# Kernel optimization log

Measured on AMD Instinct MI355X. Metric: run time of the kernel, lower is better.

## Reference

```python
import jax, jax.numpy as jnp
import numpy as np

# Tokenizer hyperparams (match init_kwargs)
NUM_VARS = 8
EMBED = 64
WIN = 16
STEP = 4
SWIDTH = 1.0  # sample_width
PWIDTH = 1.0  # patch_width
BATCH = 32
SAMPLES = 4096


def setup_inputs() -> dict:
    key = jax.random.key(0)
    k1, k2, k3, k4, k5 = jax.random.split(key, 5)
    return {
        "x": jax.random.normal(k1, (BATCH, NUM_VARS, SAMPLES), dtype=jnp.float32),
        "W1": jax.random.normal(k2, (NUM_VARS, EMBED), dtype=jnp.float32),   # sample-level LSH hyperplanes
        "b1": jax.random.normal(k3, (EMBED,), dtype=jnp.float32),
        "W2": jax.random.normal(k4, (WIN * EMBED, EMBED), dtype=jnp.float32),  # patch-level LSH hyperplanes
        "b2": jax.random.normal(k5, (EMBED,), dtype=jnp.float32),
    }


def reference(x, W1, b1, W2, b2):
    B, V, S = x.shape
    # encode(): per-timestep sample-level LSH hash, fully vectorized over S.
    # torch loop does sample_level(x[:,:,ix]) for each ix -> one batched einsum here.
    # e: [B, EMBED, S]
    e = jnp.floor((jnp.einsum('bvs,vd->bds', x, W1) + b1[None, :, None]) / SWIDTH)

    # quantize(): sliding windows over the time axis.
    starts = jnp.arange(0, S - WIN, STEP)                 # [T] window start positions
    idx = starts[:, None] + jnp.arange(WIN)[None, :]
    wins = e[:, :, idx]
    T = starts.shape[0]
    flat = wins.transpose(0, 2, 1, 3).reshape(B, T, EMBED * WIN)
    # patch-level LSH hash per window
    tokens = jnp.floor((jnp.einsum('btf,fe->bte', flat, W2) + b2) / PWIDTH)  # [B, T, EMBED]
    return tokens
```

## Files before the change

kernel.cpp:

```cpp
#include <hip/hip_runtime.h>
#include <cstdint>
#include <cstddef>

#define B_ 32
#define V_ 8
#define S_ 4096
#define E_ 64
#define T_ 1020
#define TT 32
#define SLP 200

typedef __bf16 bf16_t;
typedef bf16_t bf16x8 __attribute__((ext_vector_type(8)));
typedef float f32x4 __attribute__((ext_vector_type(4)));

__global__ __launch_bounds__(256) void prep_kernel(const float* __restrict__ W2,
                                                   bf16_t* __restrict__ w2sw) {
  const int q = blockIdx.x * 256 + threadIdx.x;
  const int l = q & 63, nt = (q >> 6) & 3, kk = q >> 8;
  const int fb = kk * 32 + (l >> 4) * 8;
  const int n = nt * 16 + (l & 15);
  bf16x8 v;
#pragma unroll
  for (int j = 0; j < 8; ++j) v[j] = (bf16_t)W2[(fb + j) * E_ + n];
  *reinterpret_cast<bf16x8*>(w2sw + (size_t)q * 8) = v;
}

__global__ __launch_bounds__(256, 4) void fused_kernel(const float* __restrict__ x,
                                                       const float* __restrict__ W1,
                                                       const float* __restrict__ b1,
                                                       const bf16_t* __restrict__ w2sw,
                                                       const float* __restrict__ b2,
                                                       float* __restrict__ out) {
  __shared__ bf16_t et[E_ * SLP];
  const int tid = threadIdx.x;
  const int b = blockIdx.y;
  const int t0 = blockIdx.x * TT;
  {
    const int dg = tid >> 5;
    const int sg = tid & 31;
    const int s0 = 4 * t0;
    float xv[V_][5];
#pragma unroll
    for (int v = 0; v < V_; ++v) {
#pragma unroll
      for (int k = 0; k < 5; ++k) {
        int s = s0 + sg + 32 * k;
        if (s > S_ - 1) s = S_ - 1;
        xv[v][k] = x[((size_t)(b * V_ + v) << 12) + s];
      }
    }
#pragma unroll
    for (int dd = 0; dd < 8; ++dd) {
      const int d = dg * 8 + dd;
      const float bb = b1[d];
      float acc[5];
#pragma unroll
      for (int k = 0; k < 5; ++k) acc[k] = bb;
#pragma unroll
      for (int v = 0; v < V_; ++v) {
        const float w = W1[v * E_ + d];
#pragma unroll
        for (int k = 0; k < 5; ++k) acc[k] += xv[v][k] * w;
      }
#pragma unroll
      for (int k = 0; k < 5; ++k)
        et[d * SLP + sg + 32 * k] = (bf16_t)floorf(acc[k]);
    }
  }
  __syncthreads();
  const int lane = tid & 63;
  const int wv = tid >> 6;
  const int l15 = lane & 15;
  const int g = lane >> 4;
  const char* etb = reinterpret_cast<const char*>(et);
  const uint32_t aoff = 400u * (g >> 1) + 8u * l15 + 16u * (g & 1);
  const bf16_t* bptr = w2sw + (((size_t)wv * 64 + lane) << 3);
  const float bv = b2[wv * 16 + l15];
  f32x4 acc0 = {bv, bv, bv, bv};
  f32x4 acc1 = {bv, bv, bv, bv};
#pragma unroll 4
  for (int kk = 0; kk < 32; ++kk) {
    const char* pa = etb + aoff + 800 * kk;
    union { uint64_t q[2]; bf16x8 v; } A0, A1;
    A0.q[0] = *reinterpret_cast<const uint64_t*>(pa);
    A0.q[1] = *reinterpret_cast<const uint64_t*>(pa + 8);
    A1.q[0] = *reinterpret_cast<const uint64_t*>(pa + 128);
    A1.q[1] = *reinterpret_cast<const uint64_t*>(pa + 136);
    const bf16x8 Bf = *reinterpret_cast<const bf16x8*>(bptr + ((size_t)kk << 11));
    acc0 = __builtin_amdgcn_mfma_f32_16x16x32_bf16(A0.v, Bf, acc0, 0, 0, 0);
    acc1 = __builtin_amdgcn_mfma_f32_16x16x32_bf16(A1.v, Bf, acc1, 0, 0, 0);
  }
#pragma unroll
  for (int r = 0; r < 4; ++r) {
    const int t1 = t0 + g * 4 + r;
    if (t1 < T_) out[((size_t)(b * T_ + t1)) * E_ + wv * 16 + l15] = floorf(acc0[r]);
    const int t2 = t0 + 16 + g * 4 + r;
    if (t2 < T_) out[((size_t)(b * T_ + t2)) * E_ + wv * 16 + l15] = floorf(acc1[r]);
  }
}

extern "C" void kernel_launch(void* const* d_in, const int* in_sizes, int n_in,
                              void* d_out, int out_size, void* d_ws, size_t ws_size,
                              hipStream_t stream) {
  const float* x  = (const float*)d_in[0];
  const float* W1 = (const float*)d_in[1];
  const float* b1 = (const float*)d_in[2];
  const float* W2 = (const float*)d_in[3];
  const float* b2 = (const float*)d_in[4];
  float* out = (float*)d_out;

  bf16_t* w2sw = (bf16_t*)d_ws;

  hipLaunchKernelGGL(prep_kernel, dim3(32), dim3(256), 0, stream, W2, w2sw);
  hipLaunchKernelGGL(fused_kernel, dim3((T_ + TT - 1) / TT, B_), dim3(256), 0, stream,
                     x, W1, b1, w2sw, b2, out);
}
```

Measured before the change: 21.35 us.

## Use 32x32x16 MFMA with split-K across waves and LDS reduction

```diff
diff --git a/kernel.cpp b/kernel.cpp
--- a/kernel.cpp
+++ b/kernel.cpp
@@ -12,14 +12,14 @@
 
 typedef __bf16 bf16_t;
 typedef bf16_t bf16x8 __attribute__((ext_vector_type(8)));
-typedef float f32x4 __attribute__((ext_vector_type(4)));
+typedef float f32x16 __attribute__((ext_vector_type(16)));
 
 __global__ __launch_bounds__(256) void prep_kernel(const float* __restrict__ W2,
                                                    bf16_t* __restrict__ w2sw) {
   const int q = blockIdx.x * 256 + threadIdx.x;
-  const int l = q & 63, nt = (q >> 6) & 3, kk = q >> 8;
-  const int fb = kk * 32 + (l >> 4) * 8;
-  const int n = nt * 16 + (l & 15);
+  const int l = q & 63, nh = (q >> 6) & 1, kk = q >> 7;
+  const int fb = 16 * kk + 8 * (l >> 5);
+  const int n = 32 * nh + (l & 31);
   bf16x8 v;
 #pragma unroll
   for (int j = 0; j < 8; ++j) v[j] = (bf16_t)W2[(fb + j) * E_ + n];
@@ -71,32 +71,44 @@
   __syncthreads();
   const int lane = tid & 63;
   const int wv = tid >> 6;
-  const int l15 = lane & 15;
-  const int g = lane >> 4;
+  const int nh = wv & 1;
+  const int kh = wv >> 1;
+  const int l31 = lane & 31;
+  const int g = lane >> 5;
   const char* etb = reinterpret_cast<const char*>(et);
-  const uint32_t aoff = 400u * (g >> 1) + 8u * l15 + 16u * (g & 1);
-  const bf16_t* bptr = w2sw + (((size_t)wv * 64 + lane) << 3);
-  const float bv = b2[wv * 16 + l15];
-  f32x4 acc0 = {bv, bv, bv, bv};
-  f32x4 acc1 = {bv, bv, bv, bv};
-#pragma unroll 4
-  for (int kk = 0; kk < 32; ++kk) {
-    const char* pa = etb + aoff + 800 * kk;
-    union { uint64_t q[2]; bf16x8 v; } A0, A1;
-    A0.q[0] = *reinterpret_cast<const uint64_t*>(pa);
-    A0.q[1] = *reinterpret_cast<const uint64_t*>(pa + 8);
-    A1.q[0] = *reinterpret_cast<const uint64_t*>(pa + 128);
-    A1.q[1] = *reinterpret_cast<const uint64_t*>(pa + 136);
-    const bf16x8 Bf = *reinterpret_cast<const bf16x8*>(bptr + ((size_t)kk << 11));
-    acc0 = __builtin_amdgcn_mfma_f32_16x16x32_bf16(A0.v, Bf, acc0, 0, 0, 0);
-    acc1 = __builtin_amdgcn_mfma_f32_16x16x32_bf16(A1.v, Bf, acc1, 0, 0, 0);
+  const uint32_t aoff = 8u * l31 + 16u * g + 400u * (kh * 32);
+  const bf16_t* bptr = w2sw + ((size_t)kh * 32768 + nh * 512 + lane * 8);
+  f32x16 acc = {};
+#pragma unroll 8
+  for (int kkl = 0; kkl < 32; ++kkl) {
+    const char* pa = etb + aoff + 400u * kkl;
+    union { uint64_t q[2]; bf16x8 v; } A;
+    A.q[0] = *reinterpret_cast<const uint64_t*>(pa);
+    A.q[1] = *reinterpret_cast<const uint64_t*>(pa + 8);
+    const bf16x8 Bf = *reinterpret_cast<const bf16x8*>(bptr + ((size_t)kkl << 10));
+    acc = __builtin_amdgcn_mfma_f32_32x32x16_bf16(A.v, Bf, acc, 0, 0, 0);
   }
+  __syncthreads();
+  float* red = reinterpret_cast<float*>(et);
+  if (kh == 1) {
 #pragma unroll
-  for (int r = 0; r < 4; ++r) {
-    const int t1 = t0 + g * 4 + r;
-    if (t1 < T_) out[((size_t)(b * T_ + t1)) * E_ + wv * 16 + l15] = floorf(acc0[r]);
-    const int t2 = t0 + 16 + g * 4 + r;
-    if (t2 < T_) out[((size_t)(b * T_ + t2)) * E_ + wv * 16 + l15] = floorf(acc1[r]);
+    for (int r = 0; r < 16; ++r) red[r * 128 + nh * 64 + lane] = acc[r];
+  }
+  __syncthreads();
+  if (kh == 0) {
+    const float bv = b2[nh * 32 + l31];
+#pragma unroll
+    for (int r = 0; r < 16; ++r) acc[r] += red[r * 128 + nh * 64 + lane];
+#pragma unroll
+    for (int q4 = 0; q4 < 4; ++q4) {
+#pragma unroll
+      for (int rr = 0; rr < 4; ++rr) {
+        const int row = q4 * 8 + rr + 4 * g;
+        const int t = t0 + row;
+        if (t < T_)
+          out[((size_t)(b * T_ + t)) * E_ + nh * 32 + l31] = floorf(acc[q4 * 4 + rr] + bv);
+      }
+    }
   }
 }
 
```

Result: slower. 22.36 us (+4.7%).

## Prefetch W2 fragments into registers before stage 1 and remap sample-hash threads

Applied to the files above, without the earlier changes.

```diff
diff --git a/kernel.cpp b/kernel.cpp
--- a/kernel.cpp
+++ b/kernel.cpp
@@ -13,6 +13,8 @@
 typedef __bf16 bf16_t;
 typedef bf16_t bf16x8 __attribute__((ext_vector_type(8)));
 typedef float f32x4 __attribute__((ext_vector_type(4)));
+typedef unsigned long long u64;
+typedef u64 u64x2 __attribute__((ext_vector_type(2)));
 
 __global__ __launch_bounds__(256) void prep_kernel(const float* __restrict__ W2,
                                                    bf16_t* __restrict__ w2sw) {
@@ -36,57 +38,80 @@
   const int tid = threadIdx.x;
   const int b = blockIdx.y;
   const int t0 = blockIdx.x * TT;
-  {
-    const int dg = tid >> 5;
-    const int sg = tid & 31;
-    const int s0 = 4 * t0;
-    float xv[V_][5];
+  const int lane = tid & 63;
+  const int wvu = __builtin_amdgcn_readfirstlane(tid >> 6);
+  const int l15 = lane & 15;
+  const int g = lane >> 4;
+  const int s0 = 4 * t0;
+
+  int sc[3];
+#pragma unroll
+  for (int k = 0; k < 3; ++k) {
+    int s = s0 + lane + 64 * k;
+    sc[k] = (s > S_ - 1) ? (S_ - 1) : s;
+  }
+  float xv[V_][3];
+#pragma unroll
+  for (int v = 0; v < V_; ++v) {
+    const float* xb = x + ((size_t)(b * V_ + v) << 12);
+#pragma unroll
+    for (int k = 0; k < 3; ++k) xv[v][k] = xb[sc[k]];
+  }
+  const bf16_t* bptr = w2sw + (((size_t)wvu * 64 + lane) << 3);
+  bf16x8 bpre[16];
+#pragma unroll
+  for (int kk = 0; kk < 16; ++kk) {
+    bpre[kk] = *reinterpret_cast<const bf16x8*>(bptr + ((size_t)kk << 11));
+    u64x2 t = __builtin_bit_cast(u64x2, bpre[kk]);
+    asm volatile("" : "+v"(t[0]), "+v"(t[1]));
+    bpre[kk] = __builtin_bit_cast(bf16x8, t);
+  }
+
+  const int dbase = wvu * 16;
+  const float* w1w = W1 + dbase;
+  const float* b1w = b1 + dbase;
+#pragma unroll
+  for (int dd = 0; dd < 16; ++dd) {
+    const float bb = b1w[dd];
+    float a0 = bb, a1 = bb, a2 = bb;
 #pragma unroll
     for (int v = 0; v < V_; ++v) {
-#pragma unroll
-      for (int k = 0; k < 5; ++k) {
-        int s = s0 + sg + 32 * k;
-        if (s > S_ - 1) s = S_ - 1;
-        xv[v][k] = x[((size_t)(b * V_ + v) << 12) + s];
-      }
+      const float w = w1w[v * E_ + dd];
+      a0 += xv[v][0] * w;
+      a1 += xv[v][1] * w;
+      a2 += xv[v][2] * w;
     }
-#pragma unroll
-    for (int dd = 0; dd < 8; ++dd) {
-      const int d = dg * 8 + dd;
-      const float bb = b1[d];
-      float acc[5];
-#pragma unroll
-      for (int k = 0; k < 5; ++k) acc[k] = bb;
-#pragma unroll
-      for (int v = 0; v < V_; ++v) {
-        const float w = W1[v * E_ + d];
-#pragma unroll
-        for (int k = 0; k < 5; ++k) acc[k] += xv[v][k] * w;
-      }
-#pragma unroll
-      for (int k = 0; k < 5; ++k)
-        et[d * SLP + sg + 32 * k] = (bf16_t)floorf(acc[k]);
-    }
+    const int row = (dbase + dd) * SLP;
+    et[row + lane]      = (bf16_t)floorf(a0);
+    et[row + lane + 64] = (bf16_t)floorf(a1);
+    if (lane < 12) et[row + lane + 128] = (bf16_t)floorf(a2);
   }
   __syncthreads();
-  const int lane = tid & 63;
-  const int wv = tid >> 6;
-  const int l15 = lane & 15;
-  const int g = lane >> 4;
+
   const char* etb = reinterpret_cast<const char*>(et);
   const uint32_t aoff = 400u * (g >> 1) + 8u * l15 + 16u * (g & 1);
-  const bf16_t* bptr = w2sw + (((size_t)wv * 64 + lane) << 3);
-  const float bv = b2[wv * 16 + l15];
+  const float bv = b2[wvu * 16 + l15];
   f32x4 acc0 = {bv, bv, bv, bv};
   f32x4 acc1 = {bv, bv, bv, bv};
-#pragma unroll 4
-  for (int kk = 0; kk < 32; ++kk) {
+#pragma unroll
+  for (int kk = 0; kk < 16; ++kk) {
     const char* pa = etb + aoff + 800 * kk;
-    union { uint64_t q[2]; bf16x8 v; } A0, A1;
-    A0.q[0] = *reinterpret_cast<const uint64_t*>(pa);
-    A0.q[1] = *reinterpret_cast<const uint64_t*>(pa + 8);
-    A1.q[0] = *reinterpret_cast<const uint64_t*>(pa + 128);
-    A1.q[1] = *reinterpret_cast<const uint64_t*>(pa + 136);
+    union { u64 q[2]; bf16x8 v; } A0, A1;
+    A0.q[0] = *reinterpret_cast<const u64*>(pa);
+    A0.q[1] = *reinterpret_cast<const u64*>(pa + 8);
+    A1.q[0] = *reinterpret_cast<const u64*>(pa + 128);
+    A1.q[1] = *reinterpret_cast<const u64*>(pa + 136);
+    acc0 = __builtin_amdgcn_mfma_f32_16x16x32_bf16(A0.v, bpre[kk], acc0, 0, 0, 0);
+    acc1 = __builtin_amdgcn_mfma_f32_16x16x32_bf16(A1.v, bpre[kk], acc1, 0, 0, 0);
+  }
+#pragma unroll 8
+  for (int kk = 16; kk < 32; ++kk) {
+    const char* pa = etb + aoff + 800 * kk;
+    union { u64 q[2]; bf16x8 v; } A0, A1;
+    A0.q[0] = *reinterpret_cast<const u64*>(pa);
+    A0.q[1] = *reinterpret_cast<const u64*>(pa + 8);
+    A1.q[0] = *reinterpret_cast<const u64*>(pa + 128);
+    A1.q[1] = *reinterpret_cast<const u64*>(pa + 136);
     const bf16x8 Bf = *reinterpret_cast<const bf16x8*>(bptr + ((size_t)kk << 11));
     acc0 = __builtin_amdgcn_mfma_f32_16x16x32_bf16(A0.v, Bf, acc0, 0, 0, 0);
     acc1 = __builtin_amdgcn_mfma_f32_16x16x32_bf16(A1.v, Bf, acc1, 0, 0, 0);
@@ -94,9 +119,13 @@
 #pragma unroll
   for (int r = 0; r < 4; ++r) {
     const int t1 = t0 + g * 4 + r;
-    if (t1 < T_) out[((size_t)(b * T_ + t1)) * E_ + wv * 16 + l15] = floorf(acc0[r]);
+    if (t1 < T_)
+      __builtin_nontemporal_store(floorf(acc0[r]),
+                                  &out[((size_t)(b * T_ + t1)) * E_ + wvu * 16 + l15]);
     const int t2 = t0 + 16 + g * 4 + r;
-    if (t2 < T_) out[((size_t)(b * T_ + t2)) * E_ + wv * 16 + l15] = floorf(acc1[r]);
+    if (t2 < T_)
+      __builtin_nontemporal_store(floorf(acc1[r]),
+                                  &out[((size_t)(b * T_ + t2)) * E_ + wvu * 16 + l15]);
   }
 }
 
```

Result: slower. 23.17 us (+8.6%).
